# Optimization experiments

Hardware: AMD Instinct MI355X
Metric: run time of the kernel (lower is better)

Reference implementation:

```python
import jax, jax.numpy as jnp
import numpy as np

B, S, D = 4, 4096, 1024

def setup_inputs() -> dict:
    key = jax.random.key(0)
    k1, k2, k3 = jax.random.split(key, 3)
    scale = 1.0 / np.sqrt(D)
    x = jax.random.normal(k1, (B, S, D), dtype=jnp.float32)
    W_qkv = jax.random.normal(k2, (3 * D, D), dtype=jnp.float32) * scale
    b_qkv = jnp.zeros((3 * D,), dtype=jnp.float32)
    W_gate = jax.random.normal(k3, (D, D), dtype=jnp.float32) * scale
    b_gate = jnp.zeros((D,), dtype=jnp.float32)
    return {"x": x, "W_qkv": W_qkv, "b_qkv": b_qkv, "W_gate": W_gate, "b_gate": b_gate}

def reference(x, W_qkv, b_qkv, W_gate, b_gate):
    # qkv projection: [B,S,3D]
    qkv = jnp.einsum('bsd,ed->bse', x, W_qkv) + b_qkv
    q, k, v = jnp.split(qkv, 3, axis=-1)  # each [B,S,D]
    # associative linear-attention state: running sum of k*v along seq
    kv_state = jnp.cumsum(k * v, axis=1)
    g = jax.nn.sigmoid(jnp.einsum('bsd,ed->bse', x, W_gate) + b_gate)
    return q * kv_state * g
```

## Files before the change

kernel.cpp:

```cpp
#include <hip/hip_runtime.h>
#include <hip/hip_bf16.h>

#define BB 4
#define SS 4096
#define DD 1024
#define MM (BB * SS)
#define KK DD
#define NN (4 * DD)

typedef __attribute__((ext_vector_type(8))) short bf16x8;
typedef __attribute__((ext_vector_type(4))) float f32x4;

__device__ __forceinline__ unsigned short f2bf(float f) {
  unsigned u = __float_as_uint(f);
  u += 0x7FFF + ((u >> 16) & 1);
  return (unsigned short)(u >> 16);
}
__device__ __forceinline__ float bf2f(unsigned short h) {
  return __uint_as_float(((unsigned)h) << 16);
}

__global__ __launch_bounds__(256) void k_convert(const float* __restrict__ src,
                                                 unsigned short* __restrict__ dst, int n4) {
  int i = blockIdx.x * blockDim.x + threadIdx.x;
  int stride = gridDim.x * blockDim.x;
  for (; i < n4; i += stride) {
    float4 v = reinterpret_cast<const float4*>(src)[i];
    ushort4 o;
    o.x = f2bf(v.x); o.y = f2bf(v.y); o.z = f2bf(v.z); o.w = f2bf(v.w);
    reinterpret_cast<ushort4*>(dst)[i] = o;
  }
}

__global__ __launch_bounds__(256) void k_convert_wperm(const float* __restrict__ Wqkv,
                                                       const float* __restrict__ Wgate,
                                                       unsigned short* __restrict__ dst) {
  int n = blockIdx.x;
  const float* src;
  if (n < 1024) {
    src = Wqkv + (size_t)n * 1024;
  } else if (n < 3072) {
    int t = (n - 1024) >> 4;
    int d = ((t >> 1) << 4) + (n & 15);
    src = Wqkv + (size_t)(1024 + ((t & 1) << 10) + d) * 1024;
  } else {
    src = Wgate + (size_t)(n - 3072) * 1024;
  }
  unsigned short* o = dst + (size_t)n * 1024;
  int i = threadIdx.x * 4;
  float4 v = *(const float4*)(src + i);
  ushort4 u;
  u.x = f2bf(v.x); u.y = f2bf(v.y); u.z = f2bf(v.z); u.w = f2bf(v.w);
  *(ushort4*)(o + i) = u;
}

#define BAR() do { asm volatile("" ::: "memory"); __builtin_amdgcn_s_barrier(); asm volatile("" ::: "memory"); } while (0)
#define VMW2() asm volatile("s_waitcnt vmcnt(2)" ::: "memory")
#define VMW0() asm volatile("s_waitcnt vmcnt(0)" ::: "memory")

__global__ __launch_bounds__(512, 2) void k_gemm2(const unsigned short* __restrict__ A,
                                                  const unsigned short* __restrict__ W,
                                                  unsigned short* __restrict__ Qd,
                                                  unsigned short* __restrict__ KVd,
                                                  unsigned short* __restrict__ Gd,
                                                  const float* __restrict__ bqkv,
                                                  const float* __restrict__ bgate) {
  __shared__ unsigned short sm[32768];

  int bid0 = blockIdx.x;
  int bid = (bid0 & 7) * 128 + (bid0 >> 3);
  int tn = bid & 15, tm = bid >> 4;
  int m0 = tm * 256, n0 = tn * 256;

  int tid = threadIdx.x, wave = tid >> 6, lane = tid & 63;
  int wm = wave >> 2, wn = wave & 3;
  int r = lane & 15, g = lane >> 4;

  const unsigned short* Ag = A + (size_t)(m0 + (tid >> 2)) * KK + (tid & 3) * 8;
  const unsigned short* Wg = W + (size_t)(n0 + (tid >> 2)) * KK + (tid & 3) * 8;

  int aoff = wm * 4096 + r * 32 + g * 8;
  int boff = 16384 + (wn >> 1) * 4096 + ((wn & 1) * 64 + r) * 32 + g * 8;

#define STAGE_A(t, h, d)                                                              \
  __builtin_amdgcn_global_load_lds(                                                   \
      (const __attribute__((address_space(1))) void*)(Ag + (size_t)(h)*131072 + (t)*32), \
      (__attribute__((address_space(3))) void*)(&sm[(d)*8192 + (h)*4096 + wave * 512]), \
      16, 0, 0)
#define STAGE_B(t, h, d)                                                              \
  __builtin_amdgcn_global_load_lds(                                                   \
      (const __attribute__((address_space(1))) void*)(Wg + (size_t)(h)*131072 + (t)*32), \
      (__attribute__((address_space(3))) void*)(&sm[16384 + (d)*8192 + (h)*4096 + wave * 512]), \
      16, 0, 0)
#define LDA(m, d) (*reinterpret_cast<const bf16x8*>(&sm[aoff + (d)*8192 + (m)*512]))
#define LDB(n, d) (*reinterpret_cast<const bf16x8*>(&sm[boff + (d)*8192 + (n)*512]))
#define MFMA(x, y, c) c = __builtin_amdgcn_mfma_f32_16x16x32_bf16(x, y, c, 0, 0, 0)

  STAGE_A(0, 0, 0); STAGE_A(0, 1, 0);
  STAGE_B(0, 0, 0); STAGE_B(0, 1, 0);
  STAGE_A(1, 0, 1); STAGE_A(1, 1, 1);
  VMW2();
  BAR();

  f32x4 acc[8][4] = {};
  bf16x8 a[8], bb0, bb1;

  for (int i = 0; i < 15; ++i) {
    int t0 = 2 * i;
#pragma unroll
    for (int m = 0; m < 8; ++m) a[m] = LDA(m, 0);
    bb0 = LDB(0, 0); bb1 = LDB(1, 0);
    STAGE_B(t0 + 1, 0, 1); STAGE_B(t0 + 1, 1, 1);
    BAR();
    __builtin_amdgcn_s_setprio(1);
#pragma unroll
    for (int m = 0; m < 8; ++m) { MFMA(a[m], bb0, acc[m][0]); MFMA(a[m], bb1, acc[m][1]); }
    __builtin_amdgcn_s_setprio(0);
    BAR();
    bb0 = LDB(2, 0); bb1 = LDB(3, 0);
    STAGE_A(t0 + 2, 0, 0); STAGE_A(t0 + 2, 1, 0);
    BAR();
    __builtin_amdgcn_s_setprio(1);
#pragma unroll
    for (int m = 0; m < 8; ++m) { MFMA(a[m], bb0, acc[m][2]); MFMA(a[m], bb1, acc[m][3]); }
    __builtin_amdgcn_s_setprio(0);
    VMW2();
    BAR();
#pragma unroll
    for (int m = 0; m < 8; ++m) a[m] = LDA(m, 1);
    bb0 = LDB(0, 1); bb1 = LDB(1, 1);
    STAGE_B(t0 + 2, 0, 0); STAGE_B(t0 + 2, 1, 0);
    BAR();
    __builtin_amdgcn_s_setprio(1);
#pragma unroll
    for (int m = 0; m < 8; ++m) { MFMA(a[m], bb0, acc[m][0]); MFMA(a[m], bb1, acc[m][1]); }
    __builtin_amdgcn_s_setprio(0);
    BAR();
    bb0 = LDB(2, 1); bb1 = LDB(3, 1);
    STAGE_A(t0 + 3, 0, 1); STAGE_A(t0 + 3, 1, 1);
    BAR();
    __builtin_amdgcn_s_setprio(1);
#pragma unroll
    for (int m = 0; m < 8; ++m) { MFMA(a[m], bb0, acc[m][2]); MFMA(a[m], bb1, acc[m][3]); }
    __builtin_amdgcn_s_setprio(0);
    VMW2();
    BAR();
  }

#pragma unroll
  for (int m = 0; m < 8; ++m) a[m] = LDA(m, 0);
  bb0 = LDB(0, 0); bb1 = LDB(1, 0);
  STAGE_B(31, 0, 1); STAGE_B(31, 1, 1);
  BAR();
#pragma unroll
  for (int m = 0; m < 8; ++m) { MFMA(a[m], bb0, acc[m][0]); MFMA(a[m], bb1, acc[m][1]); }
  BAR();
  bb0 = LDB(2, 0); bb1 = LDB(3, 0);
  BAR();
#pragma unroll
  for (int m = 0; m < 8; ++m) { MFMA(a[m], bb0, acc[m][2]); MFMA(a[m], bb1, acc[m][3]); }
  VMW0();
  BAR();
#pragma unroll
  for (int m = 0; m < 8; ++m) a[m] = LDA(m, 1);
  bb0 = LDB(0, 1); bb1 = LDB(1, 1);
  BAR();
#pragma unroll
  for (int m = 0; m < 8; ++m) { MFMA(a[m], bb0, acc[m][0]); MFMA(a[m], bb1, acc[m][1]); }
  BAR();
  bb0 = LDB(2, 1); bb1 = LDB(3, 1);
  BAR();
#pragma unroll
  for (int m = 0; m < 8; ++m) { MFMA(a[m], bb0, acc[m][2]); MFMA(a[m], bb1, acc[m][3]); }

  int growb = m0 + wm * 128 + g * 4;
  if (tn < 4) {
#pragma unroll
    for (int n = 0; n < 4; ++n) {
      int col = n0 + wn * 64 + n * 16 + r;
      float bias = bqkv[col];
#pragma unroll
      for (int m = 0; m < 8; ++m)
#pragma unroll
        for (int q = 0; q < 4; ++q)
          Qd[(size_t)(growb + m * 16 + q) * DD + col] = f2bf(acc[m][n][q] + bias);
    }
  } else if (tn < 12) {
    int cb = n0 - 1024 + wn * 64;
#pragma unroll
    for (int np = 0; np < 2; ++np) {
      int d = (cb >> 1) + np * 16 + r;
      float bk = bqkv[1024 + d], bv = bqkv[2048 + d];
#pragma unroll
      for (int m = 0; m < 8; ++m)
#pragma unroll
        for (int q = 0; q < 4; ++q) {
          float kvv = (acc[m][2 * np][q] + bk) * (acc[m][2 * np + 1][q] + bv);
          KVd[(size_t)(growb + m * 16 + q) * DD + d] = f2bf(kvv);
        }
    }
  } else {
    int cb0 = n0 - 3072;
#pragma unroll
    for (int n = 0; n < 4; ++n) {
      int c = cb0 + wn * 64 + n * 16 + r;
      float bias = bgate[c];
#pragma unroll
      for (int m = 0; m < 8; ++m)
#pragma unroll
        for (int q = 0; q < 4; ++q) {
          float gv = acc[m][n][q] + bias;
          Gd[(size_t)(growb + m * 16 + q) * DD + c] = f2bf(1.f / (1.f + __expf(-gv)));
        }
    }
  }
#undef STAGE_A
#undef STAGE_B
#undef LDA
#undef LDB
#undef MFMA
}

#define NCH 128
#define CSZ (SS / NCH)

__global__ __launch_bounds__(256) void k_pass1(const unsigned short* __restrict__ KV,
                                               float* __restrict__ part) {
  int b = blockIdx.x >> 7;
  int c = blockIdx.x & (NCH - 1);
  int d = threadIdx.x * 4;
  float a0 = 0.f, a1 = 0.f, a2 = 0.f, a3 = 0.f;
  for (int s = c * CSZ; s < (c + 1) * CSZ; ++s) {
    ushort4 kv = *(const ushort4*)&KV[(size_t)(b * SS + s) * DD + d];
    a0 += bf2f(kv.x); a1 += bf2f(kv.y); a2 += bf2f(kv.z); a3 += bf2f(kv.w);
  }
  float4 o = {a0, a1, a2, a3};
  *(float4*)&part[(size_t)(b * NCH + c) * DD + d] = o;
}

__global__ __launch_bounds__(256) void k_pass2(float* __restrict__ part) {
  int gg = blockIdx.x * blockDim.x + threadIdx.x;
  int b = gg >> 10;
  int d = gg & (DD - 1);
  float run = 0.f;
  for (int c = 0; c < NCH; ++c) {
    size_t idx = (size_t)(b * NCH + c) * DD + d;
    float t = part[idx];
    part[idx] = run;
    run += t;
  }
}

__global__ __launch_bounds__(256) void k_pass3(const unsigned short* __restrict__ Q,
                                               const unsigned short* __restrict__ KV,
                                               const unsigned short* __restrict__ G,
                                               const float* __restrict__ part,
                                               float* __restrict__ out) {
  int b = blockIdx.x >> 7;
  int c = blockIdx.x & (NCH - 1);
  int d = threadIdx.x * 4;
  float4 a = *(const float4*)&part[(size_t)(b * NCH + c) * DD + d];
  for (int s = c * CSZ; s < (c + 1) * CSZ; ++s) {
    size_t rowb = (size_t)(b * SS + s) * DD;
    ushort4 q4 = *(const ushort4*)&Q[rowb + d];
    ushort4 kv4 = *(const ushort4*)&KV[rowb + d];
    ushort4 g4 = *(const ushort4*)&G[rowb + d];
    a.x += bf2f(kv4.x); a.y += bf2f(kv4.y); a.z += bf2f(kv4.z); a.w += bf2f(kv4.w);
    float4 o;
    o.x = bf2f(q4.x) * a.x * bf2f(g4.x);
    o.y = bf2f(q4.y) * a.y * bf2f(g4.y);
    o.z = bf2f(q4.z) * a.z * bf2f(g4.z);
    o.w = bf2f(q4.w) * a.w * bf2f(g4.w);
    *(float4*)&out[rowb + d] = o;
  }
}

extern "C" void kernel_launch(void* const* d_in, const int* in_sizes, int n_in,
                              void* d_out, int out_size, void* d_ws, size_t ws_size,
                              hipStream_t stream) {
  const float* x = (const float*)d_in[0];
  const float* Wqkv = (const float*)d_in[1];
  const float* bqkv = (const float*)d_in[2];
  const float* Wgate = (const float*)d_in[3];
  const float* bgate = (const float*)d_in[4];
  float* out = (float*)d_out;

  char* ws = (char*)d_ws;
  unsigned short* xb = (unsigned short*)ws;
  unsigned short* wb = (unsigned short*)(ws + (size_t)33554432);
  unsigned short* Qd = (unsigned short*)(ws + (size_t)41943040);
  unsigned short* KVd = (unsigned short*)(ws + (size_t)75497472);
  unsigned short* Gd = (unsigned short*)(ws + (size_t)109051904);
  float* part = (float*)(ws + (size_t)142606336);

  k_convert<<<2048, 256, 0, stream>>>(x, xb, MM * KK / 4);
  k_convert_wperm<<<4096, 256, 0, stream>>>(Wqkv, Wgate, wb);

  k_gemm2<<<1024, 512, 0, stream>>>(xb, wb, Qd, KVd, Gd, bqkv, bgate);

  k_pass1<<<BB * NCH, 256, 0, stream>>>(KVd, part);
  k_pass2<<<16, 256, 0, stream>>>(part);
  k_pass3<<<BB * NCH, 256, 0, stream>>>(Qd, KVd, Gd, part, out);
}
```

Measured before the change: 326.6 us.

## Double K-tile depth with swizzled LDS and finer pipeline; fold chunk prefix into pass3

The GEMM now stages 64-wide K tiles, using 128KB of LDS in place of 64KB, with an XOR swizzle on the LDS layout to avoid bank conflicts. The main loop is split into finer phases of 16 MFMAs each, with barriers and loads interleaved, to overlap global-to-LDS staging with matrix math. The separate pass2 prefix-scan kernel is dropped, and each pass3 block sums the preceding chunk partials itself. That saves a launch and a serial scan but adds redundant reads of the partials. The doubled LDS use may lower occupancy from two blocks per CU.

```diff
diff --git a/kernel.cpp b/kernel.cpp
--- a/kernel.cpp
+++ b/kernel.cpp
@@ -54,18 +54,17 @@
   *(ushort4*)(o + i) = u;
 }
 
-#define BAR() do { asm volatile("" ::: "memory"); __builtin_amdgcn_s_barrier(); asm volatile("" ::: "memory"); } while (0)
-#define VMW2() asm volatile("s_waitcnt vmcnt(2)" ::: "memory")
+#define VMW4() asm volatile("s_waitcnt vmcnt(4)" ::: "memory")
 #define VMW0() asm volatile("s_waitcnt vmcnt(0)" ::: "memory")
 
-__global__ __launch_bounds__(512, 2) void k_gemm2(const unsigned short* __restrict__ A,
+__global__ __launch_bounds__(512, 2) void k_gemm3(const unsigned short* __restrict__ A,
                                                   const unsigned short* __restrict__ W,
                                                   unsigned short* __restrict__ Qd,
                                                   unsigned short* __restrict__ KVd,
                                                   unsigned short* __restrict__ Gd,
                                                   const float* __restrict__ bqkv,
                                                   const float* __restrict__ bgate) {
-  __shared__ unsigned short sm[32768];
+  __shared__ unsigned short sm[65536];
 
   int bid0 = blockIdx.x;
   int bid = (bid0 & 7) * 128 + (bid0 >> 3);
@@ -76,102 +75,99 @@
   int wm = wave >> 2, wn = wave & 3;
   int r = lane & 15, g = lane >> 4;
 
-  const unsigned short* Ag = A + (size_t)(m0 + (tid >> 2)) * KK + (tid & 3) * 8;
-  const unsigned short* Wg = W + (size_t)(n0 + (tid >> 2)) * KK + (tid & 3) * 8;
-
-  int aoff = wm * 4096 + r * 32 + g * 8;
-  int boff = 16384 + (wn >> 1) * 4096 + ((wn & 1) * 64 + r) * 32 + g * 8;
-
-#define STAGE_A(t, h, d)                                                              \
-  __builtin_amdgcn_global_load_lds(                                                   \
-      (const __attribute__((address_space(1))) void*)(Ag + (size_t)(h)*131072 + (t)*32), \
-      (__attribute__((address_space(3))) void*)(&sm[(d)*8192 + (h)*4096 + wave * 512]), \
-      16, 0, 0)
-#define STAGE_B(t, h, d)                                                              \
-  __builtin_amdgcn_global_load_lds(                                                   \
-      (const __attribute__((address_space(1))) void*)(Wg + (size_t)(h)*131072 + (t)*32), \
-      (__attribute__((address_space(3))) void*)(&sm[16384 + (d)*8192 + (h)*4096 + wave * 512]), \
-      16, 0, 0)
-#define LDA(m, d) (*reinterpret_cast<const bf16x8*>(&sm[aoff + (d)*8192 + (m)*512]))
-#define LDB(n, d) (*reinterpret_cast<const bf16x8*>(&sm[boff + (d)*8192 + (n)*512]))
-#define MFMA(x, y, c) c = __builtin_amdgcn_mfma_f32_16x16x32_bf16(x, y, c, 0, 0, 0)
-
-  STAGE_A(0, 0, 0); STAGE_A(0, 1, 0);
-  STAGE_B(0, 0, 0); STAGE_B(0, 1, 0);
-  STAGE_A(1, 0, 1); STAGE_A(1, 1, 1);
-  VMW2();
-  BAR();
+  int pt = tid * 16;
+  int psw = pt ^ (((pt >> 9) & 1) << 5);
+  int srow = psw >> 7;
+  int scol = (psw & 127) >> 1;
+  const unsigned short* Ag = A + (size_t)(m0 + srow) * KK + scol;
+  const unsigned short* Wg = W + (size_t)(n0 + srow) * KK + scol;
+
+#define STG_A(kt, h, d) do {                                                              \
+    __builtin_amdgcn_global_load_lds(                                                     \
+        (const __attribute__((address_space(1))) void*)(Ag + (size_t)(h)*131072 + (kt)*64), \
+        (__attribute__((address_space(3))) void*)&sm[(d)*16384 + (h)*8192 + wave*512], 16, 0, 0); \
+    __builtin_amdgcn_global_load_lds(                                                     \
+        (const __attribute__((address_space(1))) void*)(Ag + (size_t)(h)*131072 + 65536 + (kt)*64), \
+        (__attribute__((address_space(3))) void*)&sm[(d)*16384 + (h)*8192 + 4096 + wave*512], 16, 0, 0); \
+  } while (0)
+#define STG_B(kt, h, d) do {                                                              \
+    __builtin_amdgcn_global_load_lds(                                                     \
+        (const __attribute__((address_space(1))) void*)(Wg + (size_t)(h)*131072 + (kt)*64), \
+        (__attribute__((address_space(3))) void*)&sm[32768 + (d)*16384 + (h)*8192 + wave*512], 16, 0, 0); \
+    __builtin_amdgcn_global_load_lds(                                                     \
+        (const __attribute__((address_space(1))) void*)(Wg + (size_t)(h)*131072 + 65536 + (kt)*64), \
+        (__attribute__((address_space(3))) void*)&sm[32768 + (d)*16384 + (h)*8192 + 4096 + wave*512], 16, 0, 0); \
+  } while (0)
+
+  int sx = ((r >> 2) & 1) << 4;
+  int aRd = (wm * 8192 + r * 64 + g * 8) ^ sx;
+  int bRd = (32768 + (wn >> 1) * 8192 + (wn & 1) * 4096 + r * 64 + g * 8) ^ sx;
+
+#define LDSA(d, m, ks) (*reinterpret_cast<const bf16x8*>(&sm[aRd + (d)*16384 + (m)*1024 + (ks)*32]))
+#define LDSB(d, n, ks) (*reinterpret_cast<const bf16x8*>(&sm[bRd + (d)*16384 + (n)*1024 + (ks)*32]))
 
   f32x4 acc[8][4] = {};
-  bf16x8 a[8], bb0, bb1;
-
-  for (int i = 0; i < 15; ++i) {
-    int t0 = 2 * i;
-#pragma unroll
-    for (int m = 0; m < 8; ++m) a[m] = LDA(m, 0);
-    bb0 = LDB(0, 0); bb1 = LDB(1, 0);
-    STAGE_B(t0 + 1, 0, 1); STAGE_B(t0 + 1, 1, 1);
-    BAR();
-    __builtin_amdgcn_s_setprio(1);
-#pragma unroll
-    for (int m = 0; m < 8; ++m) { MFMA(a[m], bb0, acc[m][0]); MFMA(a[m], bb1, acc[m][1]); }
-    __builtin_amdgcn_s_setprio(0);
-    BAR();
-    bb0 = LDB(2, 0); bb1 = LDB(3, 0);
-    STAGE_A(t0 + 2, 0, 0); STAGE_A(t0 + 2, 1, 0);
-    BAR();
-    __builtin_amdgcn_s_setprio(1);
-#pragma unroll
-    for (int m = 0; m < 8; ++m) { MFMA(a[m], bb0, acc[m][2]); MFMA(a[m], bb1, acc[m][3]); }
-    __builtin_amdgcn_s_setprio(0);
-    VMW2();
-    BAR();
-#pragma unroll
-    for (int m = 0; m < 8; ++m) a[m] = LDA(m, 1);
-    bb0 = LDB(0, 1); bb1 = LDB(1, 1);
-    STAGE_B(t0 + 2, 0, 0); STAGE_B(t0 + 2, 1, 0);
-    BAR();
-    __builtin_amdgcn_s_setprio(1);
-#pragma unroll
-    for (int m = 0; m < 8; ++m) { MFMA(a[m], bb0, acc[m][0]); MFMA(a[m], bb1, acc[m][1]); }
-    __builtin_amdgcn_s_setprio(0);
-    BAR();
-    bb0 = LDB(2, 1); bb1 = LDB(3, 1);
-    STAGE_A(t0 + 3, 0, 1); STAGE_A(t0 + 3, 1, 1);
-    BAR();
-    __builtin_amdgcn_s_setprio(1);
-#pragma unroll
-    for (int m = 0; m < 8; ++m) { MFMA(a[m], bb0, acc[m][2]); MFMA(a[m], bb1, acc[m][3]); }
-    __builtin_amdgcn_s_setprio(0);
-    VMW2();
-    BAR();
-  }
-
-#pragma unroll
-  for (int m = 0; m < 8; ++m) a[m] = LDA(m, 0);
-  bb0 = LDB(0, 0); bb1 = LDB(1, 0);
-  STAGE_B(31, 0, 1); STAGE_B(31, 1, 1);
-  BAR();
-#pragma unroll
-  for (int m = 0; m < 8; ++m) { MFMA(a[m], bb0, acc[m][0]); MFMA(a[m], bb1, acc[m][1]); }
-  BAR();
-  bb0 = LDB(2, 0); bb1 = LDB(3, 0);
-  BAR();
-#pragma unroll
-  for (int m = 0; m < 8; ++m) { MFMA(a[m], bb0, acc[m][2]); MFMA(a[m], bb1, acc[m][3]); }
-  VMW0();
-  BAR();
-#pragma unroll
-  for (int m = 0; m < 8; ++m) a[m] = LDA(m, 1);
-  bb0 = LDB(0, 1); bb1 = LDB(1, 1);
-  BAR();
-#pragma unroll
-  for (int m = 0; m < 8; ++m) { MFMA(a[m], bb0, acc[m][0]); MFMA(a[m], bb1, acc[m][1]); }
-  BAR();
-  bb0 = LDB(2, 1); bb1 = LDB(3, 1);
-  BAR();
-#pragma unroll
-  for (int m = 0; m < 8; ++m) { MFMA(a[m], bb0, acc[m][2]); MFMA(a[m], bb1, acc[m][3]); }
+  bf16x8 a[4][2], Bn[4][2];
+
+#define RD_A(d, mb) do { _Pragma("unroll") for (int mi = 0; mi < 4; ++mi) {               \
+    _Pragma("unroll") for (int ks = 0; ks < 2; ++ks) { a[mi][ks] = LDSA(d, (mb)+mi, ks); } } } while (0)
+#define RD_B(d, nb) do { _Pragma("unroll") for (int ni = 0; ni < 2; ++ni) {               \
+    _Pragma("unroll") for (int ks = 0; ks < 2; ++ks) { Bn[(nb)+ni][ks] = LDSB(d, (nb)+ni, ks); } } } while (0)
+
+#define BARW() do { __builtin_amdgcn_s_barrier();                                         \
+    asm volatile("s_waitcnt lgkmcnt(0)" ::: "memory");                                    \
+    __builtin_amdgcn_sched_barrier(0); } while (0)
+#define ENDB() __builtin_amdgcn_s_barrier()
+
+#define MFMA16(mb, nb) do {                                                               \
+    __builtin_amdgcn_s_setprio(1);                                                        \
+    _Pragma("unroll") for (int mi = 0; mi < 4; ++mi) {                                    \
+      _Pragma("unroll") for (int ni = 0; ni < 2; ++ni) {                                  \
+        _Pragma("unroll") for (int ks = 0; ks < 2; ++ks) {                                \
+          acc[(mb)+mi][(nb)+ni] = __builtin_amdgcn_mfma_f32_16x16x32_bf16(                \
+              a[mi][ks], Bn[(nb)+ni][ks], acc[(mb)+mi][(nb)+ni], 0, 0, 0);                \
+        } } }                                                                             \
+    __builtin_amdgcn_s_setprio(0); } while (0)
+
+  STG_A(0, 0, 0); STG_A(0, 1, 0);
+  STG_B(0, 0, 0); STG_B(0, 1, 0);
+  STG_B(1, 0, 1); STG_B(1, 1, 1);
+  VMW4();
+  __builtin_amdgcn_s_barrier();
+
+  for (int i = 0; i < 7; ++i) {
+    int tb = 2 * i + 1, tc = 2 * i + 2, td = 2 * i + 3;
+    RD_A(0, 0); RD_B(0, 0); STG_A(tb, 0, 1);
+    BARW(); MFMA16(0, 0); ENDB();
+    RD_B(0, 2); STG_A(tb, 1, 1);
+    BARW(); MFMA16(0, 2); ENDB();
+    RD_A(0, 4); STG_B(tc, 0, 0);
+    BARW(); MFMA16(4, 0); ENDB();
+    STG_B(tc, 1, 0);
+    BARW(); MFMA16(4, 2); VMW4(); ENDB();
+    RD_A(1, 0); RD_B(1, 0); STG_A(tc, 0, 0);
+    BARW(); MFMA16(0, 0); ENDB();
+    RD_B(1, 2); STG_A(tc, 1, 0);
+    BARW(); MFMA16(0, 2); ENDB();
+    RD_A(1, 4); STG_B(td, 0, 1);
+    BARW(); MFMA16(4, 0); ENDB();
+    STG_B(td, 1, 1);
+    BARW(); MFMA16(4, 2); VMW4(); ENDB();
+  }
+  RD_A(0, 0); RD_B(0, 0); STG_A(15, 0, 1);
+  BARW(); MFMA16(0, 0); ENDB();
+  RD_B(0, 2); STG_A(15, 1, 1);
+  BARW(); MFMA16(0, 2); ENDB();
+  RD_A(0, 4);
+  BARW(); MFMA16(4, 0); ENDB();
+  BARW(); MFMA16(4, 2); VMW0(); ENDB();
+  RD_A(1, 0); RD_B(1, 0);
+  BARW(); MFMA16(0, 0); ENDB();
+  RD_B(1, 2);
+  BARW(); MFMA16(0, 2); ENDB();
+  RD_A(1, 4);
+  BARW(); MFMA16(4, 0); ENDB();
+  BARW(); MFMA16(4, 2);
 
   int growb = m0 + wm * 128 + g * 4;
   if (tn < 4) {
@@ -214,11 +210,15 @@
         }
     }
   }
-#undef STAGE_A
-#undef STAGE_B
-#undef LDA
-#undef LDB
-#undef MFMA
+#undef STG_A
+#undef STG_B
+#undef LDSA
+#undef LDSB
+#undef RD_A
+#undef RD_B
+#undef BARW
+#undef ENDB
+#undef MFMA16
 }
 
 #define NCH 128
@@ -238,19 +238,6 @@
   *(float4*)&part[(size_t)(b * NCH + c) * DD + d] = o;
 }
 
-__global__ __launch_bounds__(256) void k_pass2(float* __restrict__ part) {
-  int gg = blockIdx.x * blockDim.x + threadIdx.x;
-  int b = gg >> 10;
-  int d = gg & (DD - 1);
-  float run = 0.f;
-  for (int c = 0; c < NCH; ++c) {
-    size_t idx = (size_t)(b * NCH + c) * DD + d;
-    float t = part[idx];
-    part[idx] = run;
-    run += t;
-  }
-}
-
 __global__ __launch_bounds__(256) void k_pass3(const unsigned short* __restrict__ Q,
                                                const unsigned short* __restrict__ KV,
                                                const unsigned short* __restrict__ G,
@@ -259,7 +246,12 @@
   int b = blockIdx.x >> 7;
   int c = blockIdx.x & (NCH - 1);
   int d = threadIdx.x * 4;
-  float4 a = *(const float4*)&part[(size_t)(b * NCH + c) * DD + d];
+  float4 a = {0.f, 0.f, 0.f, 0.f};
+  const float* pb = &part[(size_t)b * NCH * DD + d];
+  for (int cc = 0; cc < c; ++cc) {
+    float4 p = *(const float4*)(pb + (size_t)cc * DD);
+    a.x += p.x; a.y += p.y; a.z += p.z; a.w += p.w;
+  }
   for (int s = c * CSZ; s < (c + 1) * CSZ; ++s) {
     size_t rowb = (size_t)(b * SS + s) * DD;
     ushort4 q4 = *(const ushort4*)&Q[rowb + d];
@@ -296,9 +288,8 @@
   k_convert<<<2048, 256, 0, stream>>>(x, xb, MM * KK / 4);
   k_convert_wperm<<<4096, 256, 0, stream>>>(Wqkv, Wgate, wb);
 
-  k_gemm2<<<1024, 512, 0, stream>>>(xb, wb, Qd, KVd, Gd, bqkv, bgate);
+  k_gemm3<<<1024, 512, 0, stream>>>(xb, wb, Qd, KVd, Gd, bqkv, bgate);
 
   k_pass1<<<BB * NCH, 256, 0, stream>>>(KVd, part);
-  k_pass2<<<16, 256, 0, stream>>>(part);
   k_pass3<<<BB * NCH, 256, 0, stream>>>(Qd, KVd, Gd, part, out);
 }
```

Result: slower. 337.7 us (+3.4%).
